# Optimization experiments

Measured on AMD Instinct MI355X. Metric: run time of the kernel, lower is better.

## Reference

```python
import jax, jax.numpy as jnp
import numpy as np

MARGIN = 0.3
EPS = 1e-6  # torch.nn.functional.pairwise_distance eps


def setup_inputs() -> dict:
    key = jax.random.key(0)
    k1, k2 = jax.random.split(key)
    B, D, C = 8192, 256, 512
    embeddings = jax.random.normal(k1, (B, D), dtype=jnp.float32)
    labels = jax.random.randint(k2, (B,), 0, C, dtype=jnp.int64)
    return {"embeddings": embeddings, "labels": labels}


def reference(embeddings, labels):
    B = embeddings.shape[0]
    # pairwise squared L2 via GEMM
    dot = embeddings @ embeddings.T                      # [B, B]
    sq = jnp.diag(dot)[:, None] + jnp.diag(dot)[None, :] - 2.0 * dot
    dist_sq = jnp.clip(sq, 0.0)

    same = labels[:, None] == labels[None, :]            # [B, B] bool
    eye = jnp.eye(B, dtype=bool)
    pos_mask = same & ~eye
    neg_mask = ~same

    valid = pos_mask.any(axis=1) & neg_mask.any(axis=1)  # [B]
    INF = dist_sq.max() + 1.0

    hardest_pos_idx = jnp.argmax(dist_sq * pos_mask.astype(dist_sq.dtype), axis=1)
    hardest_neg_idx = jnp.argmin(dist_sq + same.astype(dist_sq.dtype) * INF, axis=1)

    a = embeddings
    p = embeddings[hardest_pos_idx]
    n = embeddings[hardest_neg_idx]
    # torch pairwise_distance: ||x1 - x2 + eps||_2
    d_ap = jnp.linalg.norm(a - p + EPS, axis=1)
    d_an = jnp.linalg.norm(a - n + EPS, axis=1)
    per_anchor = jnp.maximum(d_ap - d_an + MARGIN, 0.0)

    v = valid.astype(per_anchor.dtype)
    n_valid = v.sum()
    loss = jnp.where(n_valid > 0, (per_anchor * v).sum() / jnp.maximum(n_valid, 1.0), 0.0)
    return loss
```

## Files before the change

### kernel.cpp

```cpp
#include <hip/hip_runtime.h>
#include <math.h>

#define NB 8192
#define ND 256
#define MARGIN_F 0.3f
#define EPS_F 1e-6f
#define BIAS_F 512.0f
#define NFIN 2048

typedef __attribute__((ext_vector_type(8))) short bf16x8;
typedef __attribute__((ext_vector_type(4))) float f32x4;

__device__ __forceinline__ unsigned short f2bf(float x) {
    unsigned int u = __float_as_uint(x);
    return (unsigned short)((u + 0x7fffu + ((u >> 16) & 1u)) >> 16);
}

__device__ __forceinline__ void gld16(const void* g, void* l) {
    __builtin_amdgcn_global_load_lds(
        (const __attribute__((address_space(1))) void*)g,
        (__attribute__((address_space(3))) void*)l, 16, 0, 0);
}

__global__ __launch_bounds__(512) void prep_k(const float* __restrict__ emb,
                                              unsigned short* __restrict__ ehi,
                                              float* __restrict__ sqnb,
                                              unsigned int* __restrict__ pos_key,
                                              unsigned int* __restrict__ neg_key) {
    __shared__ float sm[8][16];
    const int tid = threadIdx.x;
    const int tk = tid >> 6;
    const int lane = tid & 63;
    const int q = lane >> 4;
    const int lx = lane & 15;
    const int row = blockIdx.x * 16 + lx;
    const int k = tk * 32 + q * 8;

    const float4 v0 = *reinterpret_cast<const float4*>(&emb[(size_t)row * ND + k]);
    const float4 v1 = *reinterpret_cast<const float4*>(&emb[(size_t)row * ND + k + 4]);
    ushort4 h0, h1;
    h0.x = f2bf(v0.x); h0.y = f2bf(v0.y); h0.z = f2bf(v0.z); h0.w = f2bf(v0.w);
    h1.x = f2bf(v1.x); h1.y = f2bf(v1.y); h1.z = f2bf(v1.z); h1.w = f2bf(v1.w);
    *reinterpret_cast<ushort4*>(&ehi[(size_t)blockIdx.x * 4096 + tid * 8])     = h0;
    *reinterpret_cast<ushort4*>(&ehi[(size_t)blockIdx.x * 4096 + tid * 8 + 4]) = h1;

    if (tid >= 32 && tid < 48) pos_key[blockIdx.x * 16 + (tid - 32)] = 0u;
    if (tid >= 48 && tid < 64) neg_key[blockIdx.x * 16 + (tid - 48)] = 0xFFFFFFFFu;

    float s = v0.x * v0.x + v0.y * v0.y + v0.z * v0.z + v0.w * v0.w
            + v1.x * v1.x + v1.y * v1.y + v1.z * v1.z + v1.w * v1.w;
    s += __shfl_xor(s, 16, 64);
    s += __shfl_xor(s, 32, 64);
    if (q == 0) sm[tk][lx] = s;
    __syncthreads();
    if (tid < 16) {
        float t = 0.0f;
#pragma unroll
        for (int wv = 0; wv < 8; ++wv) t += sm[wv][tid];
        sqnb[blockIdx.x * 16 + tid] = t + BIAS_F;
    }
}

template <bool DIAG>
__device__ __forceinline__ void mine_tile(
        const f32x4 (&acc)[4][4], const float (&sqjc)[4], const int (&lblc)[4],
        const unsigned (&enc)[4], const int* __restrict__ lbl_i_s,
        unsigned (&pmax)[16], unsigned (&nmin)[16],
        int wr, int wc, int q, int lx) {
#pragma unroll
    for (int tr = 0; tr < 4; ++tr) {
#pragma unroll
        for (int reg = 0; reg < 4; ++reg) {
            const int r = tr * 4 + reg;
            const int rowb = wr + tr * 16 + q * 4 + reg;
            const int lab = lbl_i_s[rowb];
#pragma unroll
            for (int tc = 0; tc < 4; ++tc) {
                const float v = fmaf(-2.0f, acc[tr][tc][reg], sqjc[tc]);
                const unsigned key = (__float_as_uint(v) & 0xFFFFE000u) | enc[tc];
                const bool same = (lblc[tc] == lab);
                bool pc = same;
                if (DIAG) pc = same && ((wc + tc * 16 + lx) != rowb);
                const unsigned pk = pc ? key : 0u;
                const unsigned nk = same ? 0xFFFFFFFFu : key;
                pmax[r] = pmax[r] >= pk ? pmax[r] : pk;
                nmin[r] = nmin[r] <= nk ? nmin[r] : nk;
            }
        }
    }
}

__global__ __launch_bounds__(256, 2) void pair_k(
        const unsigned short* __restrict__ ehi, const float* __restrict__ sqnb,
        const int* __restrict__ labels,
        unsigned int* __restrict__ pos_key, unsigned int* __restrict__ neg_key) {
    __shared__ short Bsh[64 * 512];
    __shared__ int   lbl_i_s[128];

    const int tid = threadIdx.x;
    const int w = tid >> 6;
    const int lane = tid & 63;
    const int q = lane >> 4;
    const int lx = lane & 15;
    const int bid = blockIdx.x;
    const int slice = bid & 7;
    const int i_base = (bid >> 3) * 128;
    const int wr = (w & 1) * 64;
    const int wc = (w >> 1) * 64;
    const int g0 = (i_base >> 4) + (w & 1) * 4;
    const int csb = (w >> 1) * 4;

    if (tid < 128) lbl_i_s[tid] = labels[i_base + tid];

    unsigned pmax[16], nmin[16];
#pragma unroll
    for (int r = 0; r < 16; ++r) { pmax[r] = 0u; nmin[r] = 0xFFFFFFFFu; }

#pragma unroll 1
    for (int jt = 0; jt < 8; ++jt) {
        const int jb = slice * 1024 + jt * 128;
        __syncthreads();
        {
            const unsigned short* srcB = ehi + (size_t)(jb >> 4) * 4096;
#pragma unroll
            for (int p = 0; p < 16; ++p)
                gld16(srcB + ((size_t)p * 256 + tid) * 8, Bsh + (p * 256 + tid) * 8);
        }
        int lblc[4]; float sqjc[4]; unsigned enc[4];
#pragma unroll
        for (int tc = 0; tc < 4; ++tc) {
            const int colb = wc + tc * 16 + lx;
            lblc[tc] = labels[jb + colb];
            sqjc[tc] = sqnb[jb + colb];
            enc[tc] = 8191u - (unsigned)(jb + colb);
        }
        bf16x8 a0[4], a1[4];
#pragma unroll
        for (int tr = 0; tr < 4; ++tr)
            a0[tr] = *(const bf16x8*)&ehi[((size_t)(g0 + tr) * 8 + 0) * 512 + lane * 8];
        __syncthreads();

        f32x4 acc[4][4];
#pragma unroll
        for (int a = 0; a < 4; ++a)
#pragma unroll
            for (int b = 0; b < 4; ++b) acc[a][b] = (f32x4){0.f, 0.f, 0.f, 0.f};

#pragma unroll 1
        for (int kb2 = 0; kb2 < 4; ++kb2) {
            const int kbe = kb2 * 2, kbo = kbe + 1;
#pragma unroll
            for (int tr = 0; tr < 4; ++tr)
                a1[tr] = *(const bf16x8*)&ehi[((size_t)(g0 + tr) * 8 + kbo) * 512 + lane * 8];
            {
                bf16x8 bh[4];
#pragma unroll
                for (int tc = 0; tc < 4; ++tc)
                    bh[tc] = *(const bf16x8*)&Bsh[((csb + tc) * 8 + kbe) * 512 + lane * 8];
#pragma unroll
                for (int tr = 0; tr < 4; ++tr)
#pragma unroll
                    for (int tc = 0; tc < 4; ++tc)
                        acc[tr][tc] = __builtin_amdgcn_mfma_f32_16x16x32_bf16(
                            a0[tr], bh[tc], acc[tr][tc], 0, 0, 0);
            }
            const int kbn = (kbe + 2) & 7;
#pragma unroll
            for (int tr = 0; tr < 4; ++tr)
                a0[tr] = *(const bf16x8*)&ehi[((size_t)(g0 + tr) * 8 + kbn) * 512 + lane * 8];
            {
                bf16x8 bh[4];
#pragma unroll
                for (int tc = 0; tc < 4; ++tc)
                    bh[tc] = *(const bf16x8*)&Bsh[((csb + tc) * 8 + kbo) * 512 + lane * 8];
#pragma unroll
                for (int tr = 0; tr < 4; ++tr)
#pragma unroll
                    for (int tc = 0; tc < 4; ++tc)
                        acc[tr][tc] = __builtin_amdgcn_mfma_f32_16x16x32_bf16(
                            a1[tr], bh[tc], acc[tr][tc], 0, 0, 0);
            }
        }

        if (jb == i_base)
            mine_tile<true>(acc, sqjc, lblc, enc, lbl_i_s, pmax, nmin, wr, wc, q, lx);
        else
            mine_tile<false>(acc, sqjc, lblc, enc, lbl_i_s, pmax, nmin, wr, wc, q, lx);
    }

#pragma unroll
    for (int r = 0; r < 16; ++r) {
        unsigned pm = pmax[r], nm = nmin[r];
#pragma unroll
        for (int mm = 1; mm < 16; mm <<= 1) {
            const unsigned pm2 = __shfl_xor(pm, mm, 64);
            const unsigned nm2 = __shfl_xor(nm, mm, 64);
            pm = pm >= pm2 ? pm : pm2;
            nm = nm <= nm2 ? nm : nm2;
        }
        if (lx == r) {
            const int row = i_base + wr + (r >> 2) * 16 + q * 4 + (r & 3);
            atomicMax(&pos_key[row], pm);
            atomicMin(&neg_key[row], nm);
        }
    }
}

__global__ __launch_bounds__(256) void final_k(
        const float* __restrict__ emb,
        const unsigned int* __restrict__ pos_key, const unsigned int* __restrict__ neg_key,
        float* __restrict__ pbsum, float* __restrict__ pbcnt) {
    __shared__ float ssum[4], scnt[4];
    const int w = threadIdx.x >> 6;
    const int lane = threadIdx.x & 63;
    const int i = blockIdx.x * 4 + w;

    const unsigned pk = pos_key[i], nk = neg_key[i];
    const int pi = 8191 - (int)(pk & 8191u);
    const int ni = 8191 - (int)(nk & 8191u);
    const bool valid = (pk != 0u) && (nk != 0xFFFFFFFFu);

    const float4 av  = *reinterpret_cast<const float4*>(&emb[(size_t)i  * ND + lane * 4]);
    const float4 pvv = *reinterpret_cast<const float4*>(&emb[(size_t)pi * ND + lane * 4]);
    const float4 nvv = *reinterpret_cast<const float4*>(&emb[(size_t)ni * ND + lane * 4]);
    float sap, san;
    {
        const float d0 = av.x - pvv.x + EPS_F, d1 = av.y - pvv.y + EPS_F;
        const float d2 = av.z - pvv.z + EPS_F, d3 = av.w - pvv.w + EPS_F;
        sap = d0 * d0 + d1 * d1 + d2 * d2 + d3 * d3;
        const float e0 = av.x - nvv.x + EPS_F, e1 = av.y - nvv.y + EPS_F;
        const float e2 = av.z - nvv.z + EPS_F, e3 = av.w - nvv.w + EPS_F;
        san = e0 * e0 + e1 * e1 + e2 * e2 + e3 * e3;
    }
#pragma unroll
    for (int m = 32; m; m >>= 1) {
        sap += __shfl_down(sap, m, 64);
        san += __shfl_down(san, m, 64);
    }
    if (lane == 0) {
        const float per = fmaxf(sqrtf(sap) - sqrtf(san) + MARGIN_F, 0.0f);
        ssum[w] = valid ? per : 0.0f;
        scnt[w] = valid ? 1.0f : 0.0f;
    }
    __syncthreads();
    if (threadIdx.x == 0) {
        pbsum[blockIdx.x] = ssum[0] + ssum[1] + ssum[2] + ssum[3];
        pbcnt[blockIdx.x] = scnt[0] + scnt[1] + scnt[2] + scnt[3];
    }
}

__global__ __launch_bounds__(256) void reduce_k(const float* __restrict__ pbsum,
                                                const float* __restrict__ pbcnt,
                                                float* __restrict__ out) {
    __shared__ float fs[4], fc[4];
    const int tid = threadIdx.x;
    float s = 0.0f, c = 0.0f;
#pragma unroll
    for (int r = 0; r < NFIN / 256; ++r) {
        s += pbsum[r * 256 + tid];
        c += pbcnt[r * 256 + tid];
    }
#pragma unroll
    for (int m = 32; m; m >>= 1) { s += __shfl_down(s, m, 64); c += __shfl_down(c, m, 64); }
    const int wv = tid >> 6, lane = tid & 63;
    if (lane == 0) { fs[wv] = s; fc[wv] = c; }
    __syncthreads();
    if (tid == 0) {
        const float S = fs[0] + fs[1] + fs[2] + fs[3];
        const float C = fc[0] + fc[1] + fc[2] + fc[3];
        out[0] = (C > 0.0f) ? (S / fmaxf(C, 1.0f)) : 0.0f;
    }
}

extern "C" void kernel_launch(void* const* d_in, const int* in_sizes, int n_in,
                              void* d_out, int out_size, void* d_ws, size_t ws_size,
                              hipStream_t stream) {
    const float* emb = (const float*)d_in[0];
    const int* labels = (const int*)d_in[1];
    float* out = (float*)d_out;

    char* ws = (char*)d_ws;
    unsigned short* ehi = (unsigned short*)ws;
    float* sqnb = (float*)(ws + (size_t)NB * ND * 2);
    unsigned int* pos_key = (unsigned int*)(sqnb + NB);
    unsigned int* neg_key = pos_key + NB;
    float* pbsum = (float*)(neg_key + NB);
    float* pbcnt = pbsum + NFIN;

    hipLaunchKernelGGL(prep_k, dim3(NB / 16), dim3(512), 0, stream,
                       emb, ehi, sqnb, pos_key, neg_key);
    hipLaunchKernelGGL(pair_k, dim3(512), dim3(256), 0, stream,
                       ehi, sqnb, labels, pos_key, neg_key);
    hipLaunchKernelGGL(final_k, dim3(NFIN), dim3(256), 0, stream,
                       emb, pos_key, neg_key, pbsum, pbcnt);
    hipLaunchKernelGGL(reduce_k, dim3(1), dim3(256), 0, stream, pbsum, pbcnt, out);
}
```

Baseline: 117.4 us.

## Shrink pair tile to 128x64 with per-wave 32-row strips for higher occupancy

The pairwise GEMM+mining kernel changes its block tile from 128x128 to 128x64 columns. Each wave now owns 32 rows by 64 columns instead of a 64x64 quadrant, which halves the accumulators and the LDS B buffer, and launch bounds rise to 3 blocks per CU. The mining step also reduces four candidate keys in a tree before merging them into the running max/min. The trade-off is twice as many j-tile iterations with their barriers and loads, and lower MFMA reuse per B fragment.

```diff
diff --git a/kernel.cpp b/kernel.cpp
--- a/kernel.cpp
+++ b/kernel.cpp
@@ -63,38 +63,45 @@
 
 template <bool DIAG>
 __device__ __forceinline__ void mine_tile(
-        const f32x4 (&acc)[4][4], const float (&sqjc)[4], const int (&lblc)[4],
+        const f32x4 (&acc)[2][4], const float (&sqjc)[4], const int (&lblc)[4],
         const unsigned (&enc)[4], const int* __restrict__ lbl_i_s,
-        unsigned (&pmax)[16], unsigned (&nmin)[16],
-        int wr, int wc, int q, int lx) {
-#pragma unroll
-    for (int tr = 0; tr < 4; ++tr) {
+        unsigned (&pmax)[8], unsigned (&nmin)[8],
+        int i_base, int jb, int wrow, int q, int lx) {
+#pragma unroll
+    for (int tr = 0; tr < 2; ++tr) {
 #pragma unroll
         for (int reg = 0; reg < 4; ++reg) {
             const int r = tr * 4 + reg;
-            const int rowb = wr + tr * 16 + q * 4 + reg;
+            const int rowb = wrow + tr * 16 + q * 4 + reg;
             const int lab = lbl_i_s[rowb];
+            unsigned pk[4], nk[4];
 #pragma unroll
             for (int tc = 0; tc < 4; ++tc) {
                 const float v = fmaf(-2.0f, acc[tr][tc][reg], sqjc[tc]);
                 const unsigned key = (__float_as_uint(v) & 0xFFFFE000u) | enc[tc];
                 const bool same = (lblc[tc] == lab);
                 bool pc = same;
-                if (DIAG) pc = same && ((wc + tc * 16 + lx) != rowb);
-                const unsigned pk = pc ? key : 0u;
-                const unsigned nk = same ? 0xFFFFFFFFu : key;
-                pmax[r] = pmax[r] >= pk ? pmax[r] : pk;
-                nmin[r] = nmin[r] <= nk ? nmin[r] : nk;
+                if (DIAG) pc = same && ((jb + tc * 16 + lx) != (i_base + rowb));
+                pk[tc] = pc ? key : 0u;
+                nk[tc] = same ? 0xFFFFFFFFu : key;
             }
-        }
-    }
-}
-
-__global__ __launch_bounds__(256, 2) void pair_k(
+            const unsigned pa = pk[0] >= pk[1] ? pk[0] : pk[1];
+            const unsigned pb = pk[2] >= pk[3] ? pk[2] : pk[3];
+            const unsigned pm = pa >= pb ? pa : pb;
+            pmax[r] = pmax[r] >= pm ? pmax[r] : pm;
+            const unsigned na = nk[0] <= nk[1] ? nk[0] : nk[1];
+            const unsigned nb = nk[2] <= nk[3] ? nk[2] : nk[3];
+            const unsigned nm = na <= nb ? na : nb;
+            nmin[r] = nmin[r] <= nm ? nmin[r] : nm;
+        }
+    }
+}
+
+__global__ __launch_bounds__(256, 3) void pair_k(
         const unsigned short* __restrict__ ehi, const float* __restrict__ sqnb,
         const int* __restrict__ labels,
         unsigned int* __restrict__ pos_key, unsigned int* __restrict__ neg_key) {
-    __shared__ short Bsh[64 * 512];
+    __shared__ short Bsh[32 * 512];
     __shared__ int   lbl_i_s[128];
 
     const int tid = threadIdx.x;
@@ -105,44 +112,42 @@
     const int bid = blockIdx.x;
     const int slice = bid & 7;
     const int i_base = (bid >> 3) * 128;
-    const int wr = (w & 1) * 64;
-    const int wc = (w >> 1) * 64;
-    const int g0 = (i_base >> 4) + (w & 1) * 4;
-    const int csb = (w >> 1) * 4;
+    const int wrow = w * 32;
+    const int g0 = (i_base >> 4) + w * 2;
 
     if (tid < 128) lbl_i_s[tid] = labels[i_base + tid];
 
-    unsigned pmax[16], nmin[16];
-#pragma unroll
-    for (int r = 0; r < 16; ++r) { pmax[r] = 0u; nmin[r] = 0xFFFFFFFFu; }
+    unsigned pmax[8], nmin[8];
+#pragma unroll
+    for (int r = 0; r < 8; ++r) { pmax[r] = 0u; nmin[r] = 0xFFFFFFFFu; }
 
 #pragma unroll 1
-    for (int jt = 0; jt < 8; ++jt) {
-        const int jb = slice * 1024 + jt * 128;
+    for (int jt = 0; jt < 16; ++jt) {
+        const int jb = slice * 1024 + jt * 64;
         __syncthreads();
         {
             const unsigned short* srcB = ehi + (size_t)(jb >> 4) * 4096;
 #pragma unroll
-            for (int p = 0; p < 16; ++p)
+            for (int p = 0; p < 8; ++p)
                 gld16(srcB + ((size_t)p * 256 + tid) * 8, Bsh + (p * 256 + tid) * 8);
         }
         int lblc[4]; float sqjc[4]; unsigned enc[4];
 #pragma unroll
         for (int tc = 0; tc < 4; ++tc) {
-            const int colb = wc + tc * 16 + lx;
-            lblc[tc] = labels[jb + colb];
-            sqjc[tc] = sqnb[jb + colb];
-            enc[tc] = 8191u - (unsigned)(jb + colb);
-        }
-        bf16x8 a0[4], a1[4];
-#pragma unroll
-        for (int tr = 0; tr < 4; ++tr)
+            const int jj = jb + tc * 16 + lx;
+            lblc[tc] = labels[jj];
+            sqjc[tc] = sqnb[jj];
+            enc[tc] = 8191u - (unsigned)jj;
+        }
+        bf16x8 a0[2], a1[2];
+#pragma unroll
+        for (int tr = 0; tr < 2; ++tr)
             a0[tr] = *(const bf16x8*)&ehi[((size_t)(g0 + tr) * 8 + 0) * 512 + lane * 8];
         __syncthreads();
 
-        f32x4 acc[4][4];
-#pragma unroll
-        for (int a = 0; a < 4; ++a)
+        f32x4 acc[2][4];
+#pragma unroll
+        for (int a = 0; a < 2; ++a)
 #pragma unroll
             for (int b = 0; b < 4; ++b) acc[a][b] = (f32x4){0.f, 0.f, 0.f, 0.f};
 
@@ -150,15 +155,15 @@
         for (int kb2 = 0; kb2 < 4; ++kb2) {
             const int kbe = kb2 * 2, kbo = kbe + 1;
 #pragma unroll
-            for (int tr = 0; tr < 4; ++tr)
+            for (int tr = 0; tr < 2; ++tr)
                 a1[tr] = *(const bf16x8*)&ehi[((size_t)(g0 + tr) * 8 + kbo) * 512 + lane * 8];
             {
                 bf16x8 bh[4];
 #pragma unroll
                 for (int tc = 0; tc < 4; ++tc)
-                    bh[tc] = *(const bf16x8*)&Bsh[((csb + tc) * 8 + kbe) * 512 + lane * 8];
-#pragma unroll
-                for (int tr = 0; tr < 4; ++tr)
+                    bh[tc] = *(const bf16x8*)&Bsh[(tc * 8 + kbe) * 512 + lane * 8];
+#pragma unroll
+                for (int tr = 0; tr < 2; ++tr)
 #pragma unroll
                     for (int tc = 0; tc < 4; ++tc)
                         acc[tr][tc] = __builtin_amdgcn_mfma_f32_16x16x32_bf16(
@@ -166,15 +171,15 @@
             }
             const int kbn = (kbe + 2) & 7;
 #pragma unroll
-            for (int tr = 0; tr < 4; ++tr)
+            for (int tr = 0; tr < 2; ++tr)
                 a0[tr] = *(const bf16x8*)&ehi[((size_t)(g0 + tr) * 8 + kbn) * 512 + lane * 8];
             {
                 bf16x8 bh[4];
 #pragma unroll
                 for (int tc = 0; tc < 4; ++tc)
-                    bh[tc] = *(const bf16x8*)&Bsh[((csb + tc) * 8 + kbo) * 512 + lane * 8];
-#pragma unroll
-                for (int tr = 0; tr < 4; ++tr)
+                    bh[tc] = *(const bf16x8*)&Bsh[(tc * 8 + kbo) * 512 + lane * 8];
+#pragma unroll
+                for (int tr = 0; tr < 2; ++tr)
 #pragma unroll
                     for (int tc = 0; tc < 4; ++tc)
                         acc[tr][tc] = __builtin_amdgcn_mfma_f32_16x16x32_bf16(
@@ -182,14 +187,14 @@
             }
         }
 
-        if (jb == i_base)
-            mine_tile<true>(acc, sqjc, lblc, enc, lbl_i_s, pmax, nmin, wr, wc, q, lx);
+        if ((unsigned)(jb - i_base) < 128u)
+            mine_tile<true>(acc, sqjc, lblc, enc, lbl_i_s, pmax, nmin, i_base, jb, wrow, q, lx);
         else
-            mine_tile<false>(acc, sqjc, lblc, enc, lbl_i_s, pmax, nmin, wr, wc, q, lx);
-    }
-
-#pragma unroll
-    for (int r = 0; r < 16; ++r) {
+            mine_tile<false>(acc, sqjc, lblc, enc, lbl_i_s, pmax, nmin, i_base, jb, wrow, q, lx);
+    }
+
+#pragma unroll
+    for (int r = 0; r < 8; ++r) {
         unsigned pm = pmax[r], nm = nmin[r];
 #pragma unroll
         for (int mm = 1; mm < 16; mm <<= 1) {
@@ -199,7 +204,7 @@
             nm = nm <= nm2 ? nm : nm2;
         }
         if (lx == r) {
-            const int row = i_base + wr + (r >> 2) * 16 + q * 4 + (r & 3);
+            const int row = i_base + wrow + (r >> 2) * 16 + q * 4 + (r & 3);
             atomicMax(&pos_key[row], pm);
             atomicMin(&neg_key[row], nm);
         }
```

Measured after the change: 122.2 us. 1.04x slower.
